# Performance work log

Hardware: AMD Instinct MI355X
Metric: run time of the kernel (lower is better)

The kernel has to match this reference:

```python
import jax, jax.numpy as jnp
import numpy as np

H = 768; NH = 12; HD = 64; LW = 256
NEG = -1e9  # finite stand-in for -inf; exp underflows to 0 identically in fp32 softmax

def setup_inputs() -> dict:
    key = jax.random.key(0)
    ks = jax.random.split(key, 10)
    s = 0.02
    return {
        "x": jax.random.normal(ks[0], (2, 2048, H), dtype=jnp.float32),
        "w_attn": jax.random.normal(ks[1], (H, 3 * H), dtype=jnp.float32) * s,
        "b_attn": jnp.zeros((3 * H,), dtype=jnp.float32),
        "w_proj": jax.random.normal(ks[2], (H, H), dtype=jnp.float32) * s,
        "b_proj": jnp.zeros((H,), dtype=jnp.float32),
        "w_sel1": jax.random.normal(ks[3], (H, H // 4), dtype=jnp.float32) * s,
        "b_sel1": jnp.zeros((H // 4,), dtype=jnp.float32),
        "w_sel2": jax.random.normal(ks[4], (H // 4, 1), dtype=jnp.float32) * s,
        "b_sel2": jnp.zeros((1,), dtype=jnp.float32),
        "local_weight": jnp.float32(0.5),
        "global_weight": jnp.float32(0.5),
    }

def reference(x, w_attn, b_attn, w_proj, b_proj, w_sel1, b_sel1, w_sel2, b_sel2,
              local_weight, global_weight):
    B, T, C = x.shape
    scale = HD ** -0.5
    qkv = x @ w_attn + b_attn                       # [B,T,3C]
    q, k, v = jnp.split(qkv, 3, axis=-1)
    q = q.reshape(B, T, NH, HD).transpose(0, 2, 1, 3)  # [B,H,T,D]
    k = k.reshape(B, T, NH, HD).transpose(0, 2, 1, 3)
    v = v.reshape(B, T, NH, HD).transpose(0, 2, 1, 3)
    scores = jnp.einsum('bhqd,bhkd->bhqk', q, k) * scale  # [B,H,T,T]
    i = jnp.arange(T)[:, None]
    j = jnp.arange(T)[None, :]
    causal = j > i
    scores = jnp.where(causal[None, None], NEG, scores)
    # selectivity: per-key-position gate in [0.2, 1.0]
    sel = jax.nn.sigmoid(jax.nn.gelu(x @ w_sel1 + b_sel1, approximate=False) @ w_sel2 + b_sel2)  # [B,T,1]
    sel = sel[:, None, :, 0][:, :, None, :]            # [B,1,1,T]
    modulated = scores * (0.2 + 0.8 * sel)
    outside_local = j < jnp.clip(i - LW, 0, None)
    local = jnp.where(outside_local[None, None], NEG, scores)
    wl = jax.nn.sigmoid(local_weight)
    wg = jax.nn.sigmoid(global_weight)
    wsum = wl + wg
    wl, wg = wl / wsum, wg / wsum
    attn = wl * jax.nn.softmax(local, axis=-1) + wg * jax.nn.softmax(modulated, axis=-1)
    out = jnp.einsum('bhqk,bhkd->bhqd', attn, v)        # [B,H,T,D]
    out = out.transpose(0, 2, 1, 3).reshape(B, T, C)
    return out @ w_proj + b_proj
```

## Files before the change

kernel.cpp:

```cpp
#include <hip/hip_runtime.h>
#include <cmath>

#define TT    2048
#define CC    768
#define NHEAD 12
#define LWIN  256
#define BBATCH 2
#define MROWS 4096
#define QBA   128
#define KB    64
#define NSLOT 72
#define L2E   1.4426950408889634f

typedef unsigned int u32;
typedef u32 u32x2 __attribute__((ext_vector_type(2)));
typedef u32 u32x4 __attribute__((ext_vector_type(4)));
typedef short bf16x8 __attribute__((ext_vector_type(8)));
typedef float f32x16 __attribute__((ext_vector_type(16)));

union F4 { u32x4 u; bf16x8 h; };

__device__ __forceinline__ unsigned short b16(float a) {
  u32 u = __float_as_uint(a);
  return (unsigned short)((u + 0x7FFFu + ((u >> 16) & 1u)) >> 16);
}
__device__ __forceinline__ u32 pk2(float a, float b) {
  return (u32)b16(a) | ((u32)b16(b) << 16);
}

__global__ __launch_bounds__(256) void prep_kernel(
    const float* __restrict__ x, unsigned short* __restrict__ xb,
    const float* __restrict__ w_attn, unsigned short* __restrict__ wta,
    const float* __restrict__ w_proj, unsigned short* __restrict__ wtp,
    const float* __restrict__ w_sel1, unsigned short* __restrict__ wts) {
  __shared__ float t[32][33];
  const int tid = threadIdx.x;
  int b = blockIdx.x;
  if (b < 1536) {
    const int i = b * 256 + tid;
    const float4 a = *(const float4*)&x[(size_t)i * 8];
    const float4 c = *(const float4*)&x[(size_t)i * 8 + 4];
    u32x4 w = {pk2(a.x, a.y), pk2(a.z, a.w), pk2(c.x, c.y), pk2(c.z, c.w)};
    *(u32x4*)&xb[(size_t)i * 8] = w;
    return;
  }
  b -= 1536;
  const float* W;
  unsigned short* Wt;
  int N, nx;
  if (b < 1728) {
    W = w_attn; Wt = wta; N = 2304; nx = 72;
  } else if (b < 1728 + 576) {
    b -= 1728; W = w_proj; Wt = wtp; N = 768; nx = 24;
  } else {
    b -= 1728 + 576; W = w_sel1; Wt = wts; N = 192; nx = 6;
  }
  const int n0 = (b % nx) * 32, k0 = (b / nx) * 32;
  const int r = tid >> 5, c = tid & 31;
#pragma unroll
  for (int rr = 0; rr < 4; ++rr)
    t[r + 8 * rr][c] = W[(size_t)(k0 + r + 8 * rr) * N + n0 + c];
  __syncthreads();
#pragma unroll
  for (int rr = 0; rr < 4; ++rr)
    Wt[(size_t)(n0 + r + 8 * rr) * 768 + k0 + c] = b16(t[c][r + 8 * rr]);
}

template <int NT, bool OUTBF, int ACT>
__global__ __launch_bounds__(256) void gemm_mfma_kernel(
    const unsigned short* __restrict__ A, const unsigned short* __restrict__ Bt,
    const float* __restrict__ bias, void* __restrict__ Cout,
    int M, int N, int K) {
  __shared__ alignas(16) unsigned short as_[128 * 64];
  __shared__ alignas(16) unsigned short bs_[NT * 32 * 64];
  const int tid = threadIdx.x;
  const int lane = tid & 63;
  const int wv = tid >> 6;
  const int hi = lane >> 5;
  const int l31 = lane & 31;
  const int m0 = blockIdx.y * 128, n0 = blockIdx.x * (NT * 32);

  u32x4 ar[4], br[NT];

#define G_ISSUE(K0)                                                           \
  do {                                                                        \
    _Pragma("unroll") for (int i = 0; i < 4; ++i) {                           \
      const int idx = tid + (i << 8);                                         \
      const int r = idx >> 3, c = idx & 7;                                    \
      ar[i] = *(const u32x4*)&A[(size_t)(m0 + r) * K + (K0) + c * 8];         \
    }                                                                         \
    _Pragma("unroll") for (int i = 0; i < NT; ++i) {                          \
      const int idx = tid + (i << 8);                                         \
      const int r = idx >> 3, c = idx & 7;                                    \
      br[i] = *(const u32x4*)&Bt[(size_t)(n0 + r) * K + (K0) + c * 8];        \
    }                                                                         \
  } while (0)

#define G_WRITE()                                                             \
  do {                                                                        \
    _Pragma("unroll") for (int i = 0; i < 4; ++i) {                           \
      const int idx = tid + (i << 8);                                         \
      const int r = idx >> 3, c = idx & 7;                                    \
      *(u32x4*)((char*)as_ + r * 128 + ((c ^ (r & 7)) << 4)) = ar[i];         \
    }                                                                         \
    _Pragma("unroll") for (int i = 0; i < NT; ++i) {                          \
      const int idx = tid + (i << 8);                                         \
      const int r = idx >> 3, c = idx & 7;                                    \
      *(u32x4*)((char*)bs_ + r * 128 + ((c ^ (r & 7)) << 4)) = br[i];         \
    }                                                                         \
  } while (0)

  f32x16 acc[NT];
#pragma unroll
  for (int nt = 0; nt < NT; ++nt)
#pragma unroll
    for (int r = 0; r < 16; ++r) acc[nt][r] = 0.f;

  G_ISSUE(0);
  G_WRITE();
  __syncthreads();

  const int arow = wv * 32 + l31;
  for (int k0 = 0; k0 < K; k0 += 64) {
    if (k0 + 64 < K) G_ISSUE(k0 + 64);
#pragma unroll
    for (int s = 0; s < 4; ++s) {
      F4 af;
      af.u = *(const u32x4*)((const char*)as_ + arow * 128 +
                             (((2 * s + hi) ^ (arow & 7)) << 4));
#pragma unroll
      for (int nt = 0; nt < NT; ++nt) {
        F4 bf;
        bf.u = *(const u32x4*)((const char*)bs_ + (nt * 32 + l31) * 128 +
                               (((2 * s + hi) ^ (l31 & 7)) << 4));
        acc[nt] = __builtin_amdgcn_mfma_f32_32x32x16_bf16(af.h, bf.h, acc[nt], 0, 0, 0);
      }
    }
    __syncthreads();
    if (k0 + 64 < K) G_WRITE();
    __syncthreads();
  }

#pragma unroll
  for (int nt = 0; nt < NT; ++nt)
#pragma unroll
    for (int r = 0; r < 16; ++r) {
      const int m = m0 + wv * 32 + (r & 3) + 8 * (r >> 2) + 4 * hi;
      const int n = n0 + nt * 32 + l31;
      float v = acc[nt][r] + bias[n];
      if (ACT == 1) v = 0.5f * v * (1.f + erff(v * 0.70710678118654752f));
      if (OUTBF)
        ((unsigned short*)Cout)[(size_t)m * N + n] = b16(v);
      else
        ((float*)Cout)[(size_t)m * N + n] = v;
    }
#undef G_ISSUE
#undef G_WRITE
}

__global__ __launch_bounds__(256) void gate_kernel(
    const float* __restrict__ gh, const float* __restrict__ w2,
    const float* __restrict__ b2, float* __restrict__ gate) {
  const int lane = threadIdx.x & 63;
  const int row = blockIdx.x * 4 + (threadIdx.x >> 6);
  float s = 0.f;
#pragma unroll
  for (int j = 0; j < 3; ++j) {
    const int c = lane + 64 * j;
    s = fmaf(gh[(size_t)row * 192 + c], w2[c], s);
  }
#pragma unroll
  for (int off = 32; off; off >>= 1) s += __shfl_xor(s, off, 64);
  if (lane == 0) {
    const float sel = 1.f / (1.f + __expf(-(s + b2[0])));
    gate[row] = 0.125f * L2E * (0.2f + 0.8f * sel);
  }
}

__global__ __launch_bounds__(256) void attn_part_kernel(
    const unsigned short* __restrict__ qkvb, const float* __restrict__ gate8,
    unsigned short* __restrict__ part1O, unsigned short* __restrict__ part2O,
    float* __restrict__ part2ML) {
  __shared__ alignas(16) unsigned short k_s[2][KB * 64];
  __shared__ alignas(16) unsigned short vt_s[2][64 * 68];
  __shared__ float g_s[2][KB];

  const int tid = threadIdx.x;
  const int lane = tid & 63;
  const int wv = tid >> 6;
  const int hi = lane >> 5;
  const int l31 = lane & 31;
  const int vr2 = tid & 31;
  const int vc4 = tid >> 5;
  const int bh = blockIdx.y;
  const int bb = bh / NHEAD;
  const int hh = bh % NHEAD;

  u32x4 kr[2], vr[2];
  float gr = 0.f;

#define A_ISSUE(T0, WG)                                                        \
  do {                                                                         \
    _Pragma("unroll") for (int i = 0; i < 2; ++i) {                            \
      const int idx = tid + (i << 8);                                          \
      const int r = idx >> 3, c = idx & 7;                                     \
      kr[i] = *(const u32x4*)&qkvb[(size_t)(bb * TT + (T0) + r) * 2304 +       \
                                   hh * 64 + 768 + c * 8];                     \
    }                                                                          \
    {                                                                          \
      const size_t vbase = (size_t)(bb * TT + (T0) + 2 * vr2) * 2304 +         \
                           hh * 64 + 1536 + vc4 * 8;                           \
      vr[0] = *(const u32x4*)&qkvb[vbase];                                     \
      vr[1] = *(const u32x4*)&qkvb[vbase + 2304];                              \
    }                                                                          \
    if (WG && tid < KB) gr = gate8[bb * TT + (T0) + tid];                      \
  } while (0)

#define A_WRITE(KD, VD, GD, WG)                                                \
  do {                                                                         \
    _Pragma("unroll") for (int i = 0; i < 2; ++i) {                            \
      const int idx = tid + (i << 8);                                          \
      const int r = idx >> 3, c = idx & 7;                                     \
      *(u32x4*)((char*)(KD) + r * 128 + ((c ^ (r & 7)) << 4)) = kr[i];         \
    }                                                                          \
    _Pragma("unroll") for (int k = 0; k < 8; ++k) {                            \
      const int j = k >> 1;                                                    \
      const u32 a0 = vr[0][j], a1 = vr[1][j];                                  \
      const u32 val = (k & 1) ? ((a0 >> 16) | (a1 & 0xffff0000u))              \
                              : ((a0 & 0xffffu) | (a1 << 16));                 \
      *(u32*)&(VD)[(vc4 * 8 + k) * 68 + 2 * vr2] = val;                        \
    }                                                                          \
    if (WG && tid < KB) (GD)[tid] = gr;                                        \
  } while (0)

#define QK_MFMA(KC)                                                            \
  do {                                                                         \
    _Pragma("unroll") for (int s = 0; s < 4; ++s) {                            \
      const int blk = (2 * s + hi) ^ (l31 & 7);                                \
      F4 f0, f1;                                                               \
      f0.u = *(const u32x4*)((const char*)(KC) + l31 * 128 + (blk << 4));      \
      f1.u = *(const u32x4*)((const char*)(KC) + (32 + l31) * 128 + (blk << 4));\
      S0 = __builtin_amdgcn_mfma_f32_32x32x16_bf16(f0.h, qf[s], S0, 0, 0, 0);  \
      S1 = __builtin_amdgcn_mfma_f32_32x32x16_bf16(f1.h, qf[s], S1, 0, 0, 0);  \
    }                                                                          \
  } while (0)

#define V_FRAGS(VC)                                                            \
  do {                                                                         \
    const char* vb0 = (const char*)(VC) + (size_t)l31 * 136 + hi * 8;          \
    const char* vb1 = vb0 + 32 * 136;                                          \
    _Pragma("unroll") for (int kb4 = 0; kb4 < 4; ++kb4) {                      \
      const u32x2 a0 = *(const u32x2*)(vb0 + 32 * kb4);                        \
      const u32x2 a1 = *(const u32x2*)(vb0 + 32 * kb4 + 16);                   \
      va[kb4].u = (u32x4){a0.x, a0.y, a1.x, a1.y};                             \
      const u32x2 c0 = *(const u32x2*)(vb1 + 32 * kb4);                        \
      const u32x2 c1 = *(const u32x2*)(vb1 + 32 * kb4 + 16);                   \
      vbf[kb4].u = (u32x4){c0.x, c0.y, c1.x, c1.y};                            \
    }                                                                          \
  } while (0)

#define SOFTMAX_PV(M, L, OA, OB)                                               \
  do {                                                                         \
    float red[8];                                                              \
    _Pragma("unroll") for (int i = 0; i < 8; ++i)                              \
      red[i] = fmaxf(fmaxf(S0[i], S0[i + 8]), fmaxf(S1[i], S1[i + 8]));        \
    _Pragma("unroll") for (int off = 4; off; off >>= 1)                        \
      _Pragma("unroll") for (int i = 0; i < off; ++i)                          \
        red[i] = fmaxf(red[i], red[i + off]);                                  \
    const float pmax = fmaxf(red[0], __shfl_xor(red[0], 32));                  \
    const int resc = __any(pmax > M + 8.f);                                    \
    float f = 1.f;                                                             \
    if (resc) {                                                                \
      const float mn = fmaxf(M, pmax);                                         \
      f = exp2f(M - mn);                                                       \
      M = mn;                                                                  \
    }                                                                          \
    _Pragma("unroll") for (int r = 0; r < 16; ++r) {                           \
      S0[r] = exp2f(S0[r] - M);                                                \
      S1[r] = exp2f(S1[r] - M);                                                \
    }                                                                          \
    _Pragma("unroll") for (int i = 0; i < 8; ++i)                              \
      red[i] = (S0[i] + S0[i + 8]) + (S1[i] + S1[i + 8]);                      \
    _Pragma("unroll") for (int off = 4; off; off >>= 1)                        \
      _Pragma("unroll") for (int i = 0; i < off; ++i)                          \
        red[i] += red[i + off];                                                \
    const float sum = red[0] + __shfl_xor(red[0], 32);                         \
    if (resc) {                                                                \
      L = L * f + sum;                                                         \
      _Pragma("unroll") for (int r = 0; r < 16; ++r) {                         \
        const float fq = __shfl(f, (r & 3) + 8 * (r >> 2) + 4 * hi);           \
        OA[r] *= fq;                                                           \
        OB[r] *= fq;                                                           \
      }                                                                        \
    } else {                                                                   \
      L += sum;                                                                \
    }                                                                          \
    u32 Pp[16];                                                                \
    _Pragma("unroll") for (int w = 0; w < 8; ++w) {                            \
      asm("v_cvt_pk_bf16_f32 %0, %1, %2" : "=v"(Pp[w]) : "v"(S0[2 * w]), "v"(S0[2 * w + 1])); \
      asm("v_cvt_pk_bf16_f32 %0, %1, %2" : "=v"(Pp[8 + w]) : "v"(S1[2 * w]), "v"(S1[2 * w + 1])); \
    }                                                                          \
    _Pragma("unroll") for (int kb4 = 0; kb4 < 4; ++kb4) {                      \
      F4 a;                                                                    \
      a.u = (u32x4){Pp[4 * kb4 + 0], Pp[4 * kb4 + 1], Pp[4 * kb4 + 2],         \
                    Pp[4 * kb4 + 3]};                                          \
      OA = __builtin_amdgcn_mfma_f32_32x32x16_bf16(a.h, va[kb4].h, OA, 0, 0, 0);\
      OB = __builtin_amdgcn_mfma_f32_32x32x16_bf16(a.h, vbf[kb4].h, OB, 0, 0, 0);\
    }                                                                          \
  } while (0)

  if (blockIdx.x >= 16) {
    const int slot = (NSLOT - 1) - (blockIdx.x - 16);
    const int g = (slot < 2) ? 0 : (slot < 6) ? 1 : (slot < 12) ? 2 :
                  (slot < 20) ? 3 : (slot < 30) ? 4 : (slot < 42) ? 5 :
                  (slot < 56) ? 6 : 7;
    const int idxg = slot - g * (g + 1);
    const int e = (idxg >= g + 1) ? 1 : 0;
    const int qt = 2 * g + e;
    const int ch = idxg - e * (g + 1);
    const int r0 = qt * QBA;
    const int r0w = r0 + wv * 32;
    const int iq = r0w + l31;
    const int tlo = ch * 4;
    const int thi = min(tlo + 4, 2 * (qt + 1));

    bf16x8 qf[4];
    {
      const size_t qrow = (size_t)(bb * TT + r0w + l31) * 2304 + hh * 64;
#pragma unroll
      for (int s = 0; s < 4; ++s) {
        F4 f;
        f.u = *(const u32x4*)&qkvb[qrow + 16 * s + 8 * hi];
        qf[s] = f.h;
      }
    }

    float m2 = -1e30f, l2 = 0.f;
    f32x16 O2a, O2b;
#pragma unroll
    for (int r = 0; r < 16; ++r) { O2a[r] = 0.f; O2b[r] = 0.f; }

    A_ISSUE(tlo * 64, 1);
    A_WRITE(k_s[0], vt_s[0], g_s[0], 1);
    __syncthreads();

    int cur = 0;
    for (int t = tlo; t < thi; ++t) {
      const int t0 = t << 6;
      if (t + 1 < thi) A_ISSUE((t + 1) * 64, 1);
      if (t0 <= r0w + 31) {
        f32x16 S0, S1;
#pragma unroll
        for (int r = 0; r < 16; ++r) { S0[r] = 0.f; S1[r] = 0.f; }
        QK_MFMA(k_s[cur]);
        F4 va[4], vbf[4];
        V_FRAGS(vt_s[cur]);
        if (t0 + 63 <= r0w) {
#pragma unroll
          for (int r = 0; r < 16; ++r) {
            const int crow = (r & 3) + 8 * (r >> 2) + 4 * hi;
            S0[r] *= g_s[cur][crow];
            S1[r] *= g_s[cur][32 + crow];
          }
        } else {
#pragma unroll
          for (int r = 0; r < 16; ++r) {
            const int crow = (r & 3) + 8 * (r >> 2) + 4 * hi;
            const int k0 = t0 + crow;
            S0[r] = (k0 <= iq) ? S0[r] * g_s[cur][crow] : -1e30f;
            S1[r] = (k0 + 32 <= iq) ? S1[r] * g_s[cur][32 + crow] : -1e30f;
          }
        }
        SOFTMAX_PV(m2, l2, O2a, O2b);
      }
      if (t + 1 < thi) A_WRITE(k_s[cur ^ 1], vt_s[cur ^ 1], g_s[cur ^ 1], 1);
      __syncthreads();
      cur ^= 1;
    }

    const size_t srow = ((size_t)bh * NSLOT + slot) * 128 + wv * 32;
    if (hi == 0) {
      float2 ml;
      ml.x = m2;
      ml.y = l2;
      *(float2*)&part2ML[(srow + l31) * 2] = ml;
    }
#pragma unroll
    for (int r = 0; r < 16; ++r) {
      const int crow = (r & 3) + 8 * (r >> 2) + 4 * hi;
      const size_t rowi = srow + crow;
      part2O[rowi * 64 + l31]      = b16(O2a[r]);
      part2O[rowi * 64 + 32 + l31] = b16(O2b[r]);
    }
  } else {
    const int qt = blockIdx.x;
    const int r0 = qt * QBA;
    const int r0w = r0 + wv * 32;
    const int iq = r0w + l31;
    int tlo = (r0 - LWIN) >> 6;
    tlo = tlo < 0 ? 0 : tlo;
    const int thi = (r0 + QBA) >> 6;

    bf16x8 qf[4];
    {
      const size_t qrow = (size_t)(bb * TT + r0w + l31) * 2304 + hh * 64;
#pragma unroll
      for (int s = 0; s < 4; ++s) {
        F4 f;
        f.u = *(const u32x4*)&qkvb[qrow + 16 * s + 8 * hi];
        qf[s] = f.h;
      }
    }

    float m1 = -1e30f, l1 = 0.f;
    f32x16 O1a, O1b;
#pragma unroll
    for (int r = 0; r < 16; ++r) { O1a[r] = 0.f; O1b[r] = 0.f; }

    A_ISSUE(tlo * 64, 0);
    A_WRITE(k_s[0], vt_s[0], g_s[0], 0);
    __syncthreads();

    int cur = 0;
    for (int t = tlo; t < thi; ++t) {
      const int t0 = t << 6;
      if (t + 1 < thi) A_ISSUE((t + 1) * 64, 0);
      if (t0 + 63 >= r0w - LWIN && t0 <= r0w + 31) {
        f32x16 S0, S1;
#pragma unroll
        for (int r = 0; r < 16; ++r) { S0[r] = 0.f; S1[r] = 0.f; }
        QK_MFMA(k_s[cur]);
        F4 va[4], vbf[4];
        V_FRAGS(vt_s[cur]);
        if (t0 + 63 <= r0w && t0 >= r0w + 31 - LWIN) {
#pragma unroll
          for (int r = 0; r < 16; ++r) {
            S0[r] *= (0.125f * L2E);
            S1[r] *= (0.125f * L2E);
          }
        } else {
#pragma unroll
          for (int r = 0; r < 16; ++r) {
            const int crow = (r & 3) + 8 * (r >> 2) + 4 * hi;
            const int k0 = t0 + crow;
            const bool ok0 = (k0 <= iq) && (k0 + LWIN >= iq);
            const bool ok1 = (k0 + 32 <= iq) && (k0 + 32 + LWIN >= iq);
            S0[r] = ok0 ? S0[r] * (0.125f * L2E) : -1e30f;
            S1[r] = ok1 ? S1[r] * (0.125f * L2E) : -1e30f;
          }
        }
        SOFTMAX_PV(m1, l1, O1a, O1b);
      }
      if (t + 1 < thi) A_WRITE(k_s[cur ^ 1], vt_s[cur ^ 1], g_s[cur ^ 1], 0);
      __syncthreads();
      cur ^= 1;
    }

    const size_t obase = (((size_t)bh * 16 + qt) * 128 + wv * 32) * 64;
#pragma unroll
    for (int r = 0; r < 16; ++r) {
      const int crow = (r & 3) + 8 * (r >> 2) + 4 * hi;
      const float inv = 1.f / __shfl(l1, crow);
      part1O[obase + (size_t)crow * 64 + l31]      = b16(O1a[r] * inv);
      part1O[obase + (size_t)crow * 64 + 32 + l31] = b16(O1b[r] * inv);
    }
  }
#undef A_ISSUE
#undef A_WRITE
#undef QK_MFMA
#undef V_FRAGS
#undef SOFTMAX_PV
}

__global__ __launch_bounds__(256) void combine_kernel(
    const unsigned short* __restrict__ part1O,
    const unsigned short* __restrict__ part2O,
    const float* __restrict__ part2ML,
    const float* __restrict__ lwp, const float* __restrict__ gwp,
    unsigned short* __restrict__ aob) {
  const int t = blockIdx.x * 256 + threadIdx.x;
  const int d8 = t & 7;
  const int rr = t >> 3;
  const int bh = rr >> 11;
  const int qrow = rr & 2047;
  const int qt = qrow >> 7, row = qrow & 127;
  const int g = qt >> 1;
  const int sb = g * (g + 1) + (qt & 1) * (g + 1);
  const int nc = g + 1;

  float m = -1e30f, l = 0.f;
  float oa[4], ob[4];
#pragma unroll
  for (int j = 0; j < 4; ++j) { oa[j] = 0.f; ob[j] = 0.f; }

  for (int c = 0; c < nc; ++c) {
    const size_t rowi = ((size_t)bh * NSLOT + sb + c) * 128 + row;
    const float2 ml = *(const float2*)&part2ML[rowi * 2];
    const u32x4 po = *(const u32x4*)&part2O[(rowi << 6) + 8 * d8];
    const float mn = fmaxf(m, ml.x);
    const float e0 = exp2f(m - mn), e1 = exp2f(ml.x - mn);
    l = l * e0 + ml.y * e1;
#pragma unroll
    for (int j = 0; j < 4; ++j) {
      oa[j] = oa[j] * e0 + __uint_as_float(po[j] << 16) * e1;
      ob[j] = ob[j] * e0 + __uint_as_float(po[j] & 0xffff0000u) * e1;
    }
    m = mn;
  }
  const u32x4 o1p = *(const u32x4*)&part1O[((((size_t)bh * 16 + qt) * 128 + row) << 6) + 8 * d8];
  const float wlr = 1.f / (1.f + __expf(-lwp[0]));
  const float wgr = 1.f / (1.f + __expf(-gwp[0]));
  const float wl = wlr / (wlr + wgr);
  const float wg = wgr / (wlr + wgr);
  const float s2 = wg / l;
  u32x4 outw;
#pragma unroll
  for (int j = 0; j < 4; ++j) {
    const float outa = wl * __uint_as_float(o1p[j] << 16) + oa[j] * s2;
    const float outb = wl * __uint_as_float(o1p[j] & 0xffff0000u) + ob[j] * s2;
    outw[j] = pk2(outa, outb);
  }
  const int bb = bh / NHEAD, hh = bh % NHEAD;
  *(u32x4*)&aob[(size_t)(bb * TT + qrow) * CC + hh * 64 + 8 * d8] = outw;
}

extern "C" void kernel_launch(void* const* d_in, const int* in_sizes, int n_in,
                              void* d_out, int out_size, void* d_ws, size_t ws_size,
                              hipStream_t stream) {
  const float* x      = (const float*)d_in[0];
  const float* w_attn = (const float*)d_in[1];
  const float* b_attn = (const float*)d_in[2];
  const float* w_proj = (const float*)d_in[3];
  const float* b_proj = (const float*)d_in[4];
  const float* w_sel1 = (const float*)d_in[5];
  const float* b_sel1 = (const float*)d_in[6];
  const float* w_sel2 = (const float*)d_in[7];
  const float* b_sel2 = (const float*)d_in[8];
  const float* lw     = (const float*)d_in[9];
  const float* gw     = (const float*)d_in[10];
  float* out = (float*)d_out;

  unsigned short* qkvb  = (unsigned short*)d_ws;
  unsigned short* xb    = qkvb + (size_t)MROWS * 2304;
  unsigned short* wta   = xb + (size_t)MROWS * 768;
  unsigned short* wtp   = wta + (size_t)2304 * 768;
  unsigned short* wts   = wtp + (size_t)768 * 768;
  unsigned short* aob   = wts + (size_t)192 * 768;
  unsigned short* part1O = aob + (size_t)MROWS * 768;
  unsigned short* part2O = part1O + (size_t)24 * 16 * 128 * 64;
  float* gatebuf = (float*)(part2O + (size_t)24 * NSLOT * 128 * 64);
  float* part2ML = gatebuf + MROWS;
  float* ghbuf   = part2ML + (size_t)24 * NSLOT * 128 * 2;

  prep_kernel<<<3984, 256, 0, stream>>>(x, xb, w_attn, wta, w_proj, wtp,
                                        w_sel1, wts);
  gemm_mfma_kernel<2, false, 1><<<dim3(192 / 64, MROWS / 128), 256, 0, stream>>>(
      xb, wts, b_sel1, ghbuf, MROWS, 192, 768);
  gate_kernel<<<MROWS / 4, 256, 0, stream>>>(ghbuf, w_sel2, b_sel2, gatebuf);
  gemm_mfma_kernel<4, true, 0><<<dim3(2304 / 128, MROWS / 128), 256, 0, stream>>>(
      xb, wta, b_attn, qkvb, MROWS, 2304, 768);
  attn_part_kernel<<<dim3(NSLOT + 16, BBATCH * NHEAD), 256, 0, stream>>>(
      qkvb, gatebuf, part1O, part2O, part2ML);
  combine_kernel<<<(BBATCH * NHEAD * TT * 8) / 256, 256, 0, stream>>>(
      part1O, part2O, part2ML, lw, gw, aob);
  gemm_mfma_kernel<2, false, 0><<<dim3(768 / 64, MROWS / 128), 256, 0, stream>>>(
      aob, wtp, b_proj, out, MROWS, 768, 768);
}
```

Before: 135.2 us.

## Double attention query tile to 256 rows with 512-thread blocks

Raises the per-block query tile from 128 to 256 rows, processed by eight waves (512 threads) per block, and re-indexes the causal global-attention slots into a simple triangular layout of 36 slots over 8 query tiles. Each K/V tile loaded into shared memory is now reused by twice as many query rows, so global and LDS load traffic per unit of work drops and fewer partial results reach the combine kernel. The cost is half as many blocks, which may underfill the GPU, plus coarser load balance and heavier register pressure under the new launch bounds. The slots are also no longer launched in reverse order, so scheduling order changes.

```diff
diff --git a/kernel.cpp b/kernel.cpp
--- a/kernel.cpp
+++ b/kernel.cpp
@@ -7,9 +7,10 @@
 #define LWIN  256
 #define BBATCH 2
 #define MROWS 4096
-#define QBA   128
+#define QBA   256
 #define KB    64
-#define NSLOT 72
+#define NQT   8
+#define NSLOT 36
 #define L2E   1.4426950408889634f
 
 typedef unsigned int u32;
@@ -177,7 +178,7 @@
   }
 }
 
-__global__ __launch_bounds__(256) void attn_part_kernel(
+__global__ __launch_bounds__(512, 4) void attn_part_kernel(
     const unsigned short* __restrict__ qkvb, const float* __restrict__ gate8,
     unsigned short* __restrict__ part1O, unsigned short* __restrict__ part2O,
     float* __restrict__ part2ML) {
@@ -191,44 +192,43 @@
   const int hi = lane >> 5;
   const int l31 = lane & 31;
   const int vr2 = tid & 31;
-  const int vc4 = tid >> 5;
+  const int vc = tid >> 5;
   const int bh = blockIdx.y;
   const int bb = bh / NHEAD;
   const int hh = bh % NHEAD;
 
-  u32x4 kr[2], vr[2];
+  u32x4 kr;
+  u32x2 vra, vrb;
   float gr = 0.f;
 
 #define A_ISSUE(T0, WG)                                                        \
   do {                                                                         \
-    _Pragma("unroll") for (int i = 0; i < 2; ++i) {                            \
-      const int idx = tid + (i << 8);                                          \
-      const int r = idx >> 3, c = idx & 7;                                     \
-      kr[i] = *(const u32x4*)&qkvb[(size_t)(bb * TT + (T0) + r) * 2304 +       \
-                                   hh * 64 + 768 + c * 8];                     \
+    {                                                                          \
+      const int r = tid >> 3, c = tid & 7;                                     \
+      kr = *(const u32x4*)&qkvb[(size_t)(bb * TT + (T0) + r) * 2304 +          \
+                                hh * 64 + 768 + c * 8];                        \
     }                                                                          \
     {                                                                          \
       const size_t vbase = (size_t)(bb * TT + (T0) + 2 * vr2) * 2304 +         \
-                           hh * 64 + 1536 + vc4 * 8;                           \
-      vr[0] = *(const u32x4*)&qkvb[vbase];                                     \
-      vr[1] = *(const u32x4*)&qkvb[vbase + 2304];                              \
+                           hh * 64 + 1536 + vc * 4;                            \
+      vra = *(const u32x2*)&qkvb[vbase];                                       \
+      vrb = *(const u32x2*)&qkvb[vbase + 2304];                                \
     }                                                                          \
     if (WG && tid < KB) gr = gate8[bb * TT + (T0) + tid];                      \
   } while (0)
 
 #define A_WRITE(KD, VD, GD, WG)                                                \
   do {                                                                         \
-    _Pragma("unroll") for (int i = 0; i < 2; ++i) {                            \
-      const int idx = tid + (i << 8);                                          \
-      const int r = idx >> 3, c = idx & 7;                                     \
-      *(u32x4*)((char*)(KD) + r * 128 + ((c ^ (r & 7)) << 4)) = kr[i];         \
-    }                                                                          \
-    _Pragma("unroll") for (int k = 0; k < 8; ++k) {                            \
+    {                                                                          \
+      const int r = tid >> 3, c = tid & 7;                                     \
+      *(u32x4*)((char*)(KD) + r * 128 + ((c ^ (r & 7)) << 4)) = kr;            \
+    }                                                                          \
+    _Pragma("unroll") for (int k = 0; k < 4; ++k) {                            \
       const int j = k >> 1;                                                    \
-      const u32 a0 = vr[0][j], a1 = vr[1][j];                                  \
+      const u32 a0 = vra[j], a1 = vrb[j];                                      \
       const u32 val = (k & 1) ? ((a0 >> 16) | (a1 & 0xffff0000u))              \
                               : ((a0 & 0xffffu) | (a1 << 16));                 \
-      *(u32*)&(VD)[(vc4 * 8 + k) * 68 + 2 * vr2] = val;                        \
+      *(u32*)&(VD)[(vc * 4 + k) * 68 + 2 * vr2] = val;                         \
     }                                                                          \
     if (WG && tid < KB) (GD)[tid] = gr;                                        \
   } while (0)
@@ -309,20 +309,17 @@
     }                                                                          \
   } while (0)
 
-  if (blockIdx.x >= 16) {
-    const int slot = (NSLOT - 1) - (blockIdx.x - 16);
-    const int g = (slot < 2) ? 0 : (slot < 6) ? 1 : (slot < 12) ? 2 :
-                  (slot < 20) ? 3 : (slot < 30) ? 4 : (slot < 42) ? 5 :
-                  (slot < 56) ? 6 : 7;
-    const int idxg = slot - g * (g + 1);
-    const int e = (idxg >= g + 1) ? 1 : 0;
-    const int qt = 2 * g + e;
-    const int ch = idxg - e * (g + 1);
+  if (blockIdx.x >= NQT) {
+    const int slot = blockIdx.x - NQT;
+    const int qt = (slot < 1) ? 0 : (slot < 3) ? 1 : (slot < 6) ? 2 :
+                   (slot < 10) ? 3 : (slot < 15) ? 4 : (slot < 21) ? 5 :
+                   (slot < 28) ? 6 : 7;
+    const int ch = slot - qt * (qt + 1) / 2;
     const int r0 = qt * QBA;
     const int r0w = r0 + wv * 32;
     const int iq = r0w + l31;
     const int tlo = ch * 4;
-    const int thi = min(tlo + 4, 2 * (qt + 1));
+    const int thi = tlo + 4;
 
     bf16x8 qf[4];
     {
@@ -378,7 +375,7 @@
       cur ^= 1;
     }
 
-    const size_t srow = ((size_t)bh * NSLOT + slot) * 128 + wv * 32;
+    const size_t srow = ((size_t)bh * NSLOT + slot) * QBA + wv * 32;
     if (hi == 0) {
       float2 ml;
       ml.x = m2;
@@ -456,7 +453,7 @@
       cur ^= 1;
     }
 
-    const size_t obase = (((size_t)bh * 16 + qt) * 128 + wv * 32) * 64;
+    const size_t obase = (((size_t)bh * NQT + qt) * QBA + wv * 32) * 64;
 #pragma unroll
     for (int r = 0; r < 16; ++r) {
       const int crow = (r & 3) + 8 * (r >> 2) + 4 * hi;
@@ -483,10 +480,9 @@
   const int rr = t >> 3;
   const int bh = rr >> 11;
   const int qrow = rr & 2047;
-  const int qt = qrow >> 7, row = qrow & 127;
-  const int g = qt >> 1;
-  const int sb = g * (g + 1) + (qt & 1) * (g + 1);
-  const int nc = g + 1;
+  const int qt = qrow >> 8, row = qrow & 255;
+  const int sb = qt * (qt + 1) / 2;
+  const int nc = qt + 1;
 
   float m = -1e30f, l = 0.f;
   float oa[4], ob[4];
@@ -494,7 +490,7 @@
   for (int j = 0; j < 4; ++j) { oa[j] = 0.f; ob[j] = 0.f; }
 
   for (int c = 0; c < nc; ++c) {
-    const size_t rowi = ((size_t)bh * NSLOT + sb + c) * 128 + row;
+    const size_t rowi = ((size_t)bh * NSLOT + sb + c) * QBA + row;
     const float2 ml = *(const float2*)&part2ML[rowi * 2];
     const u32x4 po = *(const u32x4*)&part2O[(rowi << 6) + 8 * d8];
     const float mn = fmaxf(m, ml.x);
@@ -507,7 +503,7 @@
     }
     m = mn;
   }
-  const u32x4 o1p = *(const u32x4*)&part1O[((((size_t)bh * 16 + qt) * 128 + row) << 6) + 8 * d8];
+  const u32x4 o1p = *(const u32x4*)&part1O[((((size_t)bh * NQT + qt) * QBA + row) << 6) + 8 * d8];
   const float wlr = 1.f / (1.f + __expf(-lwp[0]));
   const float wgr = 1.f / (1.f + __expf(-gwp[0]));
   const float wl = wlr / (wlr + wgr);
@@ -547,10 +543,10 @@
   unsigned short* wts   = wtp + (size_t)768 * 768;
   unsigned short* aob   = wts + (size_t)192 * 768;
   unsigned short* part1O = aob + (size_t)MROWS * 768;
-  unsigned short* part2O = part1O + (size_t)24 * 16 * 128 * 64;
-  float* gatebuf = (float*)(part2O + (size_t)24 * NSLOT * 128 * 64);
+  unsigned short* part2O = part1O + (size_t)24 * NQT * QBA * 64;
+  float* gatebuf = (float*)(part2O + (size_t)24 * NSLOT * QBA * 64);
   float* part2ML = gatebuf + MROWS;
-  float* ghbuf   = part2ML + (size_t)24 * NSLOT * 128 * 2;
+  float* ghbuf   = part2ML + (size_t)24 * NSLOT * QBA * 2;
 
   prep_kernel<<<3984, 256, 0, stream>>>(x, xb, w_attn, wta, w_proj, wtp,
                                         w_sel1, wts);
@@ -559,7 +555,7 @@
   gate_kernel<<<MROWS / 4, 256, 0, stream>>>(ghbuf, w_sel2, b_sel2, gatebuf);
   gemm_mfma_kernel<4, true, 0><<<dim3(2304 / 128, MROWS / 128), 256, 0, stream>>>(
       xb, wta, b_attn, qkvb, MROWS, 2304, 768);
-  attn_part_kernel<<<dim3(NSLOT + 16, BBATCH * NHEAD), 256, 0, stream>>>(
+  attn_part_kernel<<<dim3(NSLOT + NQT, BBATCH * NHEAD), 512, 0, stream>>>(
       qkvb, gatebuf, part1O, part2O, part2ML);
   combine_kernel<<<(BBATCH * NHEAD * TT * 8) / 256, 256, 0, stream>>>(
       part1O, part2O, part2ML, lw, gw, aob);
```

Result: slower. 230.8 us (+70.7%).

## Fuse QKV and selector GEMMs into one launch and prescale Q

Applied to the files above, without the earlier changes.

The selector-hidden GEMM (with GELU) and the QKV GEMM are merged into a single kernel over a concatenated transposed weight matrix of 2560 columns, which removes one launch and one extra pass over x. The softmax scale times log2(e) is folded into Q when it is stored, so the attention kernel no longer multiplies scores in the unmasked path, and the gate stores the raw modulation factor. Columns 2496-2559 of the weight buffer are never written by prep and are computed then discarded, which wastes some work. Prescaling Q before bf16 rounding changes numerics slightly, and the global-branch code (not shown) must already apply scaling consistent with the new gate.

```diff
diff --git a/kernel.cpp b/kernel.cpp
--- a/kernel.cpp
+++ b/kernel.cpp
@@ -11,6 +11,7 @@
 #define KB    64
 #define NSLOT 72
 #define L2E   1.4426950408889634f
+#define QS    (0.125f * L2E)
 
 typedef unsigned int u32;
 typedef u32 u32x2 __attribute__((ext_vector_type(2)));
@@ -30,9 +31,9 @@
 
 __global__ __launch_bounds__(256) void prep_kernel(
     const float* __restrict__ x, unsigned short* __restrict__ xb,
-    const float* __restrict__ w_attn, unsigned short* __restrict__ wta,
+    const float* __restrict__ w_attn, unsigned short* __restrict__ wtm,
     const float* __restrict__ w_proj, unsigned short* __restrict__ wtp,
-    const float* __restrict__ w_sel1, unsigned short* __restrict__ wts) {
+    const float* __restrict__ w_sel1) {
   __shared__ float t[32][33];
   const int tid = threadIdx.x;
   int b = blockIdx.x;
@@ -49,11 +50,11 @@
   unsigned short* Wt;
   int N, nx;
   if (b < 1728) {
-    W = w_attn; Wt = wta; N = 2304; nx = 72;
+    W = w_attn; Wt = wtm; N = 2304; nx = 72;
   } else if (b < 1728 + 576) {
     b -= 1728; W = w_proj; Wt = wtp; N = 768; nx = 24;
   } else {
-    b -= 1728 + 576; W = w_sel1; Wt = wts; N = 192; nx = 6;
+    b -= 1728 + 576; W = w_sel1; Wt = wtm + (size_t)2304 * 768; N = 192; nx = 6;
   }
   const int n0 = (b % nx) * 32, k0 = (b / nx) * 32;
   const int r = tid >> 5, c = tid & 31;
@@ -64,6 +65,93 @@
 #pragma unroll
   for (int rr = 0; rr < 4; ++rr)
     Wt[(size_t)(n0 + r + 8 * rr) * 768 + k0 + c] = b16(t[c][r + 8 * rr]);
+}
+
+__global__ __launch_bounds__(256) void qkvsel_gemm_kernel(
+    const unsigned short* __restrict__ A, const unsigned short* __restrict__ Bt,
+    const float* __restrict__ b_attn, const float* __restrict__ b_sel1,
+    unsigned short* __restrict__ qkvb, float* __restrict__ ghbuf, int K) {
+  __shared__ alignas(16) unsigned short as_[128 * 64];
+  __shared__ alignas(16) unsigned short bs_[128 * 64];
+  const int tid = threadIdx.x;
+  const int lane = tid & 63;
+  const int wv = tid >> 6;
+  const int hi = lane >> 5;
+  const int l31 = lane & 31;
+  const int m0 = blockIdx.y * 128, n0 = blockIdx.x * 128;
+
+  u32x4 ar[4], br[4];
+
+#define G_ISSUE(K0)                                                           \
+  do {                                                                        \
+    _Pragma("unroll") for (int i = 0; i < 4; ++i) {                           \
+      const int idx = tid + (i << 8);                                         \
+      const int r = idx >> 3, c = idx & 7;                                    \
+      ar[i] = *(const u32x4*)&A[(size_t)(m0 + r) * K + (K0) + c * 8];         \
+      br[i] = *(const u32x4*)&Bt[(size_t)(n0 + r) * K + (K0) + c * 8];        \
+    }                                                                         \
+  } while (0)
+
+#define G_WRITE()                                                             \
+  do {                                                                        \
+    _Pragma("unroll") for (int i = 0; i < 4; ++i) {                           \
+      const int idx = tid + (i << 8);                                         \
+      const int r = idx >> 3, c = idx & 7;                                    \
+      *(u32x4*)((char*)as_ + r * 128 + ((c ^ (r & 7)) << 4)) = ar[i];         \
+      *(u32x4*)((char*)bs_ + r * 128 + ((c ^ (r & 7)) << 4)) = br[i];         \
+    }                                                                         \
+  } while (0)
+
+  f32x16 acc[4];
+#pragma unroll
+  for (int nt = 0; nt < 4; ++nt)
+#pragma unroll
+    for (int r = 0; r < 16; ++r) acc[nt][r] = 0.f;
+
+  G_ISSUE(0);
+  G_WRITE();
+  __syncthreads();
+
+  const int arow = wv * 32 + l31;
+  for (int k0 = 0; k0 < K; k0 += 64) {
+    if (k0 + 64 < K) G_ISSUE(k0 + 64);
+#pragma unroll
+    for (int s = 0; s < 4; ++s) {
+      F4 af;
+      af.u = *(const u32x4*)((const char*)as_ + arow * 128 +
+                             (((2 * s + hi) ^ (arow & 7)) << 4));
+#pragma unroll
+      for (int nt = 0; nt < 4; ++nt) {
+        F4 bf;
+        bf.u = *(const u32x4*)((const char*)bs_ + (nt * 32 + l31) * 128 +
+                               (((2 * s + hi) ^ (l31 & 7)) << 4));
+        acc[nt] = __builtin_amdgcn_mfma_f32_32x32x16_bf16(af.h, bf.h, acc[nt], 0, 0, 0);
+      }
+    }
+    __syncthreads();
+    if (k0 + 64 < K) G_WRITE();
+    __syncthreads();
+  }
+
+#pragma unroll
+  for (int nt = 0; nt < 4; ++nt)
+#pragma unroll
+    for (int r = 0; r < 16; ++r) {
+      const int m = m0 + wv * 32 + (r & 3) + 8 * (r >> 2) + 4 * hi;
+      const int n = n0 + nt * 32 + l31;
+      const float v = acc[nt][r];
+      if (n < 768) {
+        qkvb[(size_t)m * 2304 + n] = b16((v + b_attn[n]) * QS);
+      } else if (n < 2304) {
+        qkvb[(size_t)m * 2304 + n] = b16(v + b_attn[n]);
+      } else if (n < 2496) {
+        const float h = v + b_sel1[n - 2304];
+        ghbuf[(size_t)m * 192 + (n - 2304)] =
+            0.5f * h * (1.f + erff(h * 0.70710678118654752f));
+      }
+    }
+#undef G_ISSUE
+#undef G_WRITE
 }
 
 template <int NT, bool OUTBF, int ACT>
@@ -173,7 +261,7 @@
   for (int off = 32; off; off >>= 1) s += __shfl_xor(s, off, 64);
   if (lane == 0) {
     const float sel = 1.f / (1.f + __expf(-(s + b2[0])));
-    gate[row] = 0.125f * L2E * (0.2f + 0.8f * sel);
+    gate[row] = 0.2f + 0.8f * sel;
   }
 }
 
@@ -432,21 +520,15 @@
         QK_MFMA(k_s[cur]);
         F4 va[4], vbf[4];
         V_FRAGS(vt_s[cur]);
-        if (t0 + 63 <= r0w && t0 >= r0w + 31 - LWIN) {
-#pragma unroll
-          for (int r = 0; r < 16; ++r) {
-            S0[r] *= (0.125f * L2E);
-            S1[r] *= (0.125f * L2E);
-          }
-        } else {
+        if (!(t0 + 63 <= r0w && t0 >= r0w + 31 - LWIN)) {
 #pragma unroll
           for (int r = 0; r < 16; ++r) {
             const int crow = (r & 3) + 8 * (r >> 2) + 4 * hi;
             const int k0 = t0 + crow;
             const bool ok0 = (k0 <= iq) && (k0 + LWIN >= iq);
             const bool ok1 = (k0 + 32 <= iq) && (k0 + 32 + LWIN >= iq);
-            S0[r] = ok0 ? S0[r] * (0.125f * L2E) : -1e30f;
-            S1[r] = ok1 ? S1[r] * (0.125f * L2E) : -1e30f;
+            S0[r] = ok0 ? S0[r] : -1e30f;
+            S1[r] = ok1 ? S1[r] : -1e30f;
           }
         }
         SOFTMAX_PV(m1, l1, O1a, O1b);
@@ -542,23 +624,19 @@
 
   unsigned short* qkvb  = (unsigned short*)d_ws;
   unsigned short* xb    = qkvb + (size_t)MROWS * 2304;
-  unsigned short* wta   = xb + (size_t)MROWS * 768;
-  unsigned short* wtp   = wta + (size_t)2304 * 768;
-  unsigned short* wts   = wtp + (size_t)768 * 768;
-  unsigned short* aob   = wts + (size_t)192 * 768;
+  unsigned short* wtm   = xb + (size_t)MROWS * 768;
+  unsigned short* wtp   = wtm + (size_t)2560 * 768;
+  unsigned short* aob   = wtp + (size_t)768 * 768;
   unsigned short* part1O = aob + (size_t)MROWS * 768;
   unsigned short* part2O = part1O + (size_t)24 * 16 * 128 * 64;
   float* gatebuf = (float*)(part2O + (size_t)24 * NSLOT * 128 * 64);
   float* part2ML = gatebuf + MROWS;
   float* ghbuf   = part2ML + (size_t)24 * NSLOT * 128 * 2;
 
-  prep_kernel<<<3984, 256, 0, stream>>>(x, xb, w_attn, wta, w_proj, wtp,
-                                        w_sel1, wts);
-  gemm_mfma_kernel<2, false, 1><<<dim3(192 / 64, MROWS / 128), 256, 0, stream>>>(
-      xb, wts, b_sel1, ghbuf, MROWS, 192, 768);
+  prep_kernel<<<3984, 256, 0, stream>>>(x, xb, w_attn, wtm, w_proj, wtp, w_sel1);
+  qkvsel_gemm_kernel<<<dim3(2560 / 128, MROWS / 128), 256, 0, stream>>>(
+      xb, wtm, b_attn, b_sel1, qkvb, ghbuf, 768);
   gate_kernel<<<MROWS / 4, 256, 0, stream>>>(ghbuf, w_sel2, b_sel2, gatebuf);
-  gemm_mfma_kernel<4, true, 0><<<dim3(2304 / 128, MROWS / 128), 256, 0, stream>>>(
-      xb, wta, b_attn, qkvb, MROWS, 2304, 768);
   attn_part_kernel<<<dim3(NSLOT + 16, BBATCH * NHEAD), 256, 0, stream>>>(
       qkvb, gatebuf, part1O, part2O, part2ML);
   combine_kernel<<<(BBATCH * NHEAD * TT * 8) / 256, 256, 0, stream>>>(
```

New measurement: 171.8 us. +27.1%, slower.
